# Performance work log

Measured on AMD Instinct MI355X. Metric: run time of the kernel, lower is better.

Reference implementation:

```python
import jax, jax.numpy as jnp
import numpy as np

B, L, D = 2048, 128, 256
NEG_SLOPE = 0.2   # GAT-style leaky relu slope
LN_EPS = 1e-5
NEG_INF = -1e9


def setup_inputs() -> dict:
    key = jax.random.key(0)
    ks = jax.random.split(key, 10)
    mol_atom_feature = jax.random.normal(ks[0], (B, D), jnp.float32)
    atom_feature = jax.random.normal(ks[1], (B, L, D), jnp.float32)
    # attend mask: 0/1 per atom; softmax mask: 0 where attended, -1e9 where padded
    attend = jax.random.randint(ks[2], (B, L, 1), 0, 2).astype(jnp.float32)
    softmax_mask = (attend - 1.0) * (-NEG_INF)  # 0 -> -1e9... careful: (0-1)*(1e9) = -1e9? compute: (attend-1)*1e9 gives -1e9 for 0, 0 for 1
    softmax_mask = (attend - 1.0) * 1e9
    s = 1.0 / np.sqrt(D)
    W1 = jax.random.normal(ks[3], (D, D), jnp.float32) * s
    b1 = jnp.zeros((D,), jnp.float32)
    W2 = jax.random.normal(ks[4], (D, D), jnp.float32) * s
    b2 = jnp.zeros((D,), jnp.float32)
    w_align = jax.random.normal(ks[5], (D, 1), jnp.float32) * s
    b_align = jnp.zeros((1,), jnp.float32)
    ln_gamma = jnp.ones((D,), jnp.float32)
    ln_beta = jnp.zeros((D,), jnp.float32)
    return {
        "mol_atom_feature": mol_atom_feature,
        "atom_feature": atom_feature,
        "mol_atom_attend_mask": attend,
        "mol_atom_softmax_mask": softmax_mask,
        "W1": W1, "b1": b1, "W2": W2, "b2": b2,
        "w_align": w_align, "b_align": b_align,
        "ln_gamma": ln_gamma, "ln_beta": ln_beta,
    }


def _leaky_relu(x):
    return jnp.where(x >= 0, x, NEG_SLOPE * x)


def reference(mol_atom_feature, atom_feature, mol_atom_attend_mask, mol_atom_softmax_mask,
              W1, b1, W2, b2, w_align, b_align, ln_gamma, ln_beta):
    # linear transforms (dropout is identity in eval)
    q = mol_atom_feature @ W1.T + b1                      # [B, D]
    nb = atom_feature @ W2.T + b2                         # [B, L, D]
    # GATv2: act(q + neighbor) -> scalar score
    align = _leaky_relu(q[:, None, :] + nb)               # [B, L, D]
    score = align @ w_align + b_align                     # [B, L, 1]
    score = score + mol_atom_softmax_mask
    attn = jax.nn.softmax(score, axis=-2)                 # softmax over atoms L
    attn = attn * mol_atom_attend_mask
    ctx = jnp.sum(attn * nb, axis=-2)                     # [B, D]
    # LayerNorm over feature dim
    mu = jnp.mean(ctx, axis=-1, keepdims=True)
    var = jnp.mean((ctx - mu) ** 2, axis=-1, keepdims=True)
    return (ctx - mu) / jnp.sqrt(var + LN_EPS) * ln_gamma + ln_beta
```

## Files before the change

kernel.cpp:

```cpp
#include <hip/hip_runtime.h>

#define NBMOL 2048
#define NL 128
#define ND 256

constexpr float NEG_SLOPE = 0.2f;
constexpr float LN_EPS = 1e-5f;

typedef __attribute__((ext_vector_type(8))) short short8;
typedef __attribute__((ext_vector_type(4))) float f32x4;

__device__ __forceinline__ unsigned short f2bf(float f) {
  unsigned int u = __float_as_uint(f);
  u = (u + 0x7FFFu + ((u >> 16) & 1u)) >> 16;
  return (unsigned short)u;
}
__device__ __forceinline__ float bf2f(unsigned short h) {
  return __uint_as_float(((unsigned int)h) << 16);
}
__device__ __forceinline__ int swz(int row, int kbyte) {
  return row * 512 + (kbyte ^ ((row & 7) << 4));
}

__global__ __launch_bounds__(256) void pack_w2_kernel(const float* __restrict__ W2,
                                                      unsigned short* __restrict__ w2f,
                                                      unsigned short* __restrict__ w2p) {
  int g = blockIdx.x * 256 + threadIdx.x;
  int ks = g >> 10;
  int nt = (g >> 6) & 15;
  int l  = g & 63;
  int row = (l & 15) + nt * 16;
  int kb  = ((l >> 4) << 3) + ks * 32;
  const float* src = W2 + row * 256 + kb;
  unsigned short h[8];
#pragma unroll
  for (int j = 0; j < 8; ++j) h[j] = f2bf(src[j]);
  unsigned short* dst = w2f + (size_t)g * 8;
#pragma unroll
  for (int j = 0; j < 8; ++j) dst[j] = h[j];
  unsigned short* dst2 = w2p + (size_t)row * 256 + kb;
#pragma unroll
  for (int j = 0; j < 8; ++j) dst2[j] = h[j];
}

__global__ __launch_bounds__(256) void compute_q_kernel(const float* __restrict__ mol,
                                                        const float* __restrict__ W1,
                                                        const float* __restrict__ b1,
                                                        float* __restrict__ q) {
  __shared__ float mol_s[8][ND];
  const int t = threadIdx.x;
  const int b0 = blockIdx.x * 8;
#pragma unroll
  for (int i = 0; i < 8; ++i) mol_s[i][t] = mol[(size_t)(b0 + i) * ND + t];
  __syncthreads();
  float acc[8];
#pragma unroll
  for (int i = 0; i < 8; ++i) acc[i] = 0.f;
  const float4* wrow = (const float4*)(W1 + (size_t)t * ND);
  for (int k4 = 0; k4 < 64; ++k4) {
    float4 w = wrow[k4];
#pragma unroll
    for (int bb = 0; bb < 8; ++bb) {
      float4 m = *(const float4*)&mol_s[bb][k4 * 4];
      acc[bb] += w.x * m.x + w.y * m.y + w.z * m.z + w.w * m.w;
    }
  }
  float bias = b1[t];
#pragma unroll
  for (int bb = 0; bb < 8; ++bb) q[(size_t)(b0 + bb) * ND + t] = acc[bb] + bias;
}

__global__ __launch_bounds__(512, 4) void fused_kernel(
    const float* __restrict__ atom,
    const float* __restrict__ attend,
    const float* __restrict__ smask,
    const float* __restrict__ w_align,
    const float* __restrict__ b_align,
    const float* __restrict__ b2,
    const float* __restrict__ gamma_,
    const float* __restrict__ beta_,
    const unsigned short* __restrict__ w2f,
    const unsigned short* __restrict__ w2p,
    const float* __restrict__ qbuf,
    float* __restrict__ out)
{
  __shared__ unsigned short Abuf[NL * ND];
  __shared__ float sp_s[4][NL];
  __shared__ float attn_s[NL];
  __shared__ float ctx4_s[4][ND];
  __shared__ float y_s[ND];
  __shared__ float gemv_s[2][ND];
  __shared__ float red_s[2][4];
  __shared__ float t_s;

  const int tid  = threadIdx.x;
  const int lane = tid & 63;
  const int wid  = tid >> 6;
  const int wr   = wid >> 2;
  const int wc   = wid & 3;
  const int b    = blockIdx.x;

  {
    const float4* src = (const float4*)(atom + (size_t)b * (NL * ND));
#pragma unroll
    for (int half = 0; half < 2; ++half) {
      float4 v[8];
#pragma unroll
      for (int i = 0; i < 8; ++i) v[i] = src[(half * 8 + i) * 512 + tid];
#pragma unroll
      for (int i = 0; i < 8; ++i) {
        int f = (half * 8 + i) * 512 + tid;
        int row = f >> 6;
        int kbyte = (f & 63) * 8;
        ushort4 hv;
        hv.x = f2bf(v[i].x); hv.y = f2bf(v[i].y);
        hv.z = f2bf(v[i].z); hv.w = f2bf(v[i].w);
        *(ushort4*)((char*)Abuf + swz(row, kbyte)) = hv;
      }
    }
  }
  __syncthreads();

  f32x4 acc[4][4];
#pragma unroll
  for (int mm = 0; mm < 4; ++mm)
#pragma unroll
    for (int nn = 0; nn < 4; ++nn) acc[mm][nn] = {0.f, 0.f, 0.f, 0.f};

#pragma unroll
  for (int ks = 0; ks < 8; ++ks) {
    short8 bfr[4], afr[4];
#pragma unroll
    for (int nn = 0; nn < 4; ++nn) {
      const unsigned short* srcb =
          w2f + ((size_t)((ks * 16 + (wc * 4 + nn)) * 64 + lane)) * 8;
      bfr[nn] = *(const short8*)srcb;
    }
#pragma unroll
    for (int mm = 0; mm < 4; ++mm) {
      int row = wr * 64 + mm * 16 + (lane & 15);
      int kbyte = ((lane >> 4) << 4) + ks * 64;
      afr[mm] = *(const short8*)((const char*)Abuf + swz(row, kbyte));
    }
#pragma unroll
    for (int mm = 0; mm < 4; ++mm)
#pragma unroll
      for (int nn = 0; nn < 4; ++nn)
        acc[mm][nn] = __builtin_amdgcn_mfma_f32_16x16x32_bf16(
            afr[mm], bfr[nn], acc[mm][nn], 0, 0, 0);
  }

  {
    float qv[4], wv[4], bv[4];
    const float* qrow = qbuf + (size_t)b * ND;
#pragma unroll
    for (int nn = 0; nn < 4; ++nn) {
      int col = wc * 64 + nn * 16 + (lane & 15);
      qv[nn] = qrow[col];
      wv[nn] = w_align[col];
      bv[nn] = b2[col];
    }
#pragma unroll
    for (int mm = 0; mm < 4; ++mm) {
#pragma unroll
      for (int r = 0; r < 4; ++r) {
        float s = 0.f;
#pragma unroll
        for (int nn = 0; nn < 4; ++nn) {
          float t2 = qv[nn] + acc[mm][nn][r] + bv[nn];
          s += (t2 >= 0.f ? t2 : NEG_SLOPE * t2) * wv[nn];
        }
        s += __shfl_xor(s, 1);
        s += __shfl_xor(s, 2);
        s += __shfl_xor(s, 4);
        s += __shfl_xor(s, 8);
        if ((lane & 15) == 0)
          sp_s[wc][wr * 64 + mm * 16 + ((lane >> 4) << 2) + r] = s;
      }
    }
  }
  __syncthreads();

  if (wid == 0) {
    const float ba = b_align[0];
    float s0 = sp_s[0][lane] + sp_s[1][lane] + sp_s[2][lane] + sp_s[3][lane]
               + ba + smask[(size_t)b * NL + lane];
    int l1 = lane + 64;
    float s1 = sp_s[0][l1] + sp_s[1][l1] + sp_s[2][l1] + sp_s[3][l1]
               + ba + smask[(size_t)b * NL + l1];
    float m = fmaxf(s0, s1);
#pragma unroll
    for (int o = 32; o > 0; o >>= 1) m = fmaxf(m, __shfl_xor(m, o));
    float e0 = expf(s0 - m), e1 = expf(s1 - m);
    float sum = e0 + e1;
#pragma unroll
    for (int o = 32; o > 0; o >>= 1) sum += __shfl_xor(sum, o);
    float inv = 1.f / sum;
    float a0 = e0 * inv * attend[(size_t)b * NL + lane];
    float a1 = e1 * inv * attend[(size_t)b * NL + l1];
    attn_s[lane] = a0;
    attn_s[l1]   = a1;
    float tl = a0 + a1;
#pragma unroll
    for (int o = 32; o > 0; o >>= 1) tl += __shfl_xor(tl, o);
    if (lane == 0) t_s = tl;
  }
  __syncthreads();

  {
    const int d2 = tid & 127;
    const int h  = tid >> 7;
    float s0 = 0.f, s1 = 0.f;
#pragma unroll 8
    for (int li = 0; li < 32; ++li) {
      int l = h * 32 + li;
      unsigned int v = *(const unsigned int*)((const char*)Abuf + swz(l, d2 * 4));
      float a = attn_s[l];
      s0 += a * bf2f((unsigned short)(v & 0xffffu));
      s1 += a * bf2f((unsigned short)(v >> 16));
    }
    *(float2*)&ctx4_s[h][2 * d2] = make_float2(s0, s1);
  }
  __syncthreads();
  if (tid < ND)
    y_s[tid] = ctx4_s[0][tid] + ctx4_s[1][tid] + ctx4_s[2][tid] + ctx4_s[3][tid];
  __syncthreads();

  {
    const int dp = tid & 255;
    const int kh = tid >> 8;
    const unsigned short* wrow = w2p + (size_t)dp * 256 + kh * 128;
    float s = 0.f;
#pragma unroll
    for (int k8 = 0; k8 < 16; ++k8) {
      short8 w8 = *(const short8*)(wrow + k8 * 8);
      const float* yy = &y_s[kh * 128 + k8 * 8];
#pragma unroll
      for (int j = 0; j < 8; ++j)
        s += bf2f((unsigned short)w8[j]) * yy[j];
    }
    gemv_s[kh][dp] = s;
  }
  __syncthreads();

  if (tid < ND) {
    float v = gemv_s[0][tid] + gemv_s[1][tid] + t_s * b2[tid];
    float sv = v, sq = v * v;
#pragma unroll
    for (int o = 32; o > 0; o >>= 1) {
      sv += __shfl_xor(sv, o);
      sq += __shfl_xor(sq, o);
    }
    if (lane == 0) { red_s[0][wid] = sv; red_s[1][wid] = sq; }
  }
  __syncthreads();
  if (tid < ND) {
    float v = gemv_s[0][tid] + gemv_s[1][tid] + t_s * b2[tid];
    float sv = red_s[0][0] + red_s[0][1] + red_s[0][2] + red_s[0][3];
    float sq = red_s[1][0] + red_s[1][1] + red_s[1][2] + red_s[1][3];
    float mu = sv * (1.0f / 256.0f);
    float var = fmaxf(sq * (1.0f / 256.0f) - mu * mu, 0.f);
    out[(size_t)b * ND + tid] =
        (v - mu) * rsqrtf(var + LN_EPS) * gamma_[tid] + beta_[tid];
  }
}

extern "C" void kernel_launch(void* const* d_in, const int* in_sizes, int n_in,
                              void* d_out, int out_size, void* d_ws, size_t ws_size,
                              hipStream_t stream) {
  const float* mol     = (const float*)d_in[0];
  const float* atom    = (const float*)d_in[1];
  const float* attend  = (const float*)d_in[2];
  const float* smask   = (const float*)d_in[3];
  const float* W1      = (const float*)d_in[4];
  const float* b1      = (const float*)d_in[5];
  const float* W2      = (const float*)d_in[6];
  const float* b2      = (const float*)d_in[7];
  const float* w_align = (const float*)d_in[8];
  const float* b_align = (const float*)d_in[9];
  const float* gamma_  = (const float*)d_in[10];
  const float* beta_   = (const float*)d_in[11];
  float* out = (float*)d_out;

  float* qbuf = (float*)d_ws;
  unsigned short* w2f = (unsigned short*)((char*)d_ws + (size_t)NBMOL * ND * 4);
  unsigned short* w2p = w2f + 65536;

  pack_w2_kernel<<<32, 256, 0, stream>>>(W2, w2f, w2p);
  compute_q_kernel<<<256, 256, 0, stream>>>(mol, W1, b1, qbuf);
  fused_kernel<<<NBMOL, 512, 0, stream>>>(atom, attend, smask, w_align, b_align,
                                          b2, gamma_, beta_, w2f, w2p, qbuf, out);
}
```

Measured before the change: 458.2 us.

## Compute context from MFMA accumulators and stream atom tiles directly from global

The LDS staging of the whole bf16 atom tile is removed. A fragments are now loaded straight from global fp32 and packed to bf16 in registers. The context vector is formed as the attention-weighted sum of the existing MFMA accumulators (atom·W2ᵀ), which replaces the second pass over atom plus the separate W2 GEMV. The constant b_align is dropped because softmax is shift-invariant. This frees about 64KB of LDS per block and removes redundant work, but the strided per-lane global fp32 loads may coalesce less well than the old cooperative load.

```diff
diff --git a/kernel.cpp b/kernel.cpp
--- a/kernel.cpp
+++ b/kernel.cpp
@@ -1,4 +1,5 @@
 #include <hip/hip_runtime.h>
+#include <hip/hip_bf16.h>
 
 #define NBMOL 2048
 #define NL 128
@@ -15,16 +16,15 @@
   u = (u + 0x7FFFu + ((u >> 16) & 1u)) >> 16;
   return (unsigned short)u;
 }
-__device__ __forceinline__ float bf2f(unsigned short h) {
-  return __uint_as_float(((unsigned int)h) << 16);
-}
-__device__ __forceinline__ int swz(int row, int kbyte) {
-  return row * 512 + (kbyte ^ ((row & 7) << 4));
+__device__ __forceinline__ unsigned int pk2(float lo, float hi) {
+  __hip_bfloat162 h = __float22bfloat162_rn(make_float2(lo, hi));
+  unsigned int u;
+  __builtin_memcpy(&u, &h, 4);
+  return u;
 }
 
 __global__ __launch_bounds__(256) void pack_w2_kernel(const float* __restrict__ W2,
-                                                      unsigned short* __restrict__ w2f,
-                                                      unsigned short* __restrict__ w2p) {
+                                                      unsigned short* __restrict__ w2f) {
   int g = blockIdx.x * 256 + threadIdx.x;
   int ks = g >> 10;
   int nt = (g >> 6) & 15;
@@ -38,9 +38,6 @@
   unsigned short* dst = w2f + (size_t)g * 8;
 #pragma unroll
   for (int j = 0; j < 8; ++j) dst[j] = h[j];
-  unsigned short* dst2 = w2p + (size_t)row * 256 + kb;
-#pragma unroll
-  for (int j = 0; j < 8; ++j) dst2[j] = h[j];
 }
 
 __global__ __launch_bounds__(256) void compute_q_kernel(const float* __restrict__ mol,
@@ -75,21 +72,16 @@
     const float* __restrict__ attend,
     const float* __restrict__ smask,
     const float* __restrict__ w_align,
-    const float* __restrict__ b_align,
     const float* __restrict__ b2,
     const float* __restrict__ gamma_,
     const float* __restrict__ beta_,
     const unsigned short* __restrict__ w2f,
-    const unsigned short* __restrict__ w2p,
     const float* __restrict__ qbuf,
     float* __restrict__ out)
 {
-  __shared__ unsigned short Abuf[NL * ND];
-  __shared__ float sp_s[4][NL];
-  __shared__ float attn_s[NL];
-  __shared__ float ctx4_s[4][ND];
-  __shared__ float y_s[ND];
-  __shared__ float gemv_s[2][ND];
+  __shared__ float __align__(16) sp_s[4][NL];
+  __shared__ float __align__(16) attn_s[NL];
+  __shared__ float cw_s[2][ND];
   __shared__ float red_s[2][4];
   __shared__ float t_s;
 
@@ -100,47 +92,32 @@
   const int wc   = wid & 3;
   const int b    = blockIdx.x;
 
-  {
-    const float4* src = (const float4*)(atom + (size_t)b * (NL * ND));
-#pragma unroll
-    for (int half = 0; half < 2; ++half) {
-      float4 v[8];
-#pragma unroll
-      for (int i = 0; i < 8; ++i) v[i] = src[(half * 8 + i) * 512 + tid];
-#pragma unroll
-      for (int i = 0; i < 8; ++i) {
-        int f = (half * 8 + i) * 512 + tid;
-        int row = f >> 6;
-        int kbyte = (f & 63) * 8;
-        ushort4 hv;
-        hv.x = f2bf(v[i].x); hv.y = f2bf(v[i].y);
-        hv.z = f2bf(v[i].z); hv.w = f2bf(v[i].w);
-        *(ushort4*)((char*)Abuf + swz(row, kbyte)) = hv;
-      }
-    }
-  }
-  __syncthreads();
-
   f32x4 acc[4][4];
 #pragma unroll
   for (int mm = 0; mm < 4; ++mm)
 #pragma unroll
     for (int nn = 0; nn < 4; ++nn) acc[mm][nn] = {0.f, 0.f, 0.f, 0.f};
 
+  const float* abase = atom + (size_t)b * (NL * ND)
+                     + (size_t)(wr * 64 + (lane & 15)) * ND + ((lane >> 4) << 3);
+  const unsigned short* bbase = w2f + (size_t)((wc * 4) * 64 + lane) * 8;
+
 #pragma unroll
   for (int ks = 0; ks < 8; ++ks) {
-    short8 bfr[4], afr[4];
-#pragma unroll
-    for (int nn = 0; nn < 4; ++nn) {
-      const unsigned short* srcb =
-          w2f + ((size_t)((ks * 16 + (wc * 4 + nn)) * 64 + lane)) * 8;
-      bfr[nn] = *(const short8*)srcb;
-    }
+    short8 bfr[4];
+#pragma unroll
+    for (int nn = 0; nn < 4; ++nn)
+      bfr[nn] = *(const short8*)(bbase + ((size_t)(ks * 16 + nn) * 64) * 8);
+    short8 afr[4];
 #pragma unroll
     for (int mm = 0; mm < 4; ++mm) {
-      int row = wr * 64 + mm * 16 + (lane & 15);
-      int kbyte = ((lane >> 4) << 4) + ks * 64;
-      afr[mm] = *(const short8*)((const char*)Abuf + swz(row, kbyte));
+      const float* ap = abase + mm * 16 * ND + ks * 32;
+      float4 a0 = *(const float4*)ap;
+      float4 a1 = *(const float4*)(ap + 4);
+      union { unsigned int u[4]; short8 s; } f;
+      f.u[0] = pk2(a0.x, a0.y); f.u[1] = pk2(a0.z, a0.w);
+      f.u[2] = pk2(a1.x, a1.y); f.u[3] = pk2(a1.z, a1.w);
+      afr[mm] = f.s;
     }
 #pragma unroll
     for (int mm = 0; mm < 4; ++mm)
@@ -182,12 +159,11 @@
   __syncthreads();
 
   if (wid == 0) {
-    const float ba = b_align[0];
     float s0 = sp_s[0][lane] + sp_s[1][lane] + sp_s[2][lane] + sp_s[3][lane]
-               + ba + smask[(size_t)b * NL + lane];
+               + smask[(size_t)b * NL + lane];
     int l1 = lane + 64;
     float s1 = sp_s[0][l1] + sp_s[1][l1] + sp_s[2][l1] + sp_s[3][l1]
-               + ba + smask[(size_t)b * NL + l1];
+               + smask[(size_t)b * NL + l1];
     float m = fmaxf(s0, s1);
 #pragma unroll
     for (int o = 32; o > 0; o >>= 1) m = fmaxf(m, __shfl_xor(m, o));
@@ -208,43 +184,31 @@
   __syncthreads();
 
   {
-    const int d2 = tid & 127;
-    const int h  = tid >> 7;
-    float s0 = 0.f, s1 = 0.f;
-#pragma unroll 8
-    for (int li = 0; li < 32; ++li) {
-      int l = h * 32 + li;
-      unsigned int v = *(const unsigned int*)((const char*)Abuf + swz(l, d2 * 4));
-      float a = attn_s[l];
-      s0 += a * bf2f((unsigned short)(v & 0xffffu));
-      s1 += a * bf2f((unsigned short)(v >> 16));
-    }
-    *(float2*)&ctx4_s[h][2 * d2] = make_float2(s0, s1);
-  }
-  __syncthreads();
-  if (tid < ND)
-    y_s[tid] = ctx4_s[0][tid] + ctx4_s[1][tid] + ctx4_s[2][tid] + ctx4_s[3][tid];
-  __syncthreads();
-
-  {
-    const int dp = tid & 255;
-    const int kh = tid >> 8;
-    const unsigned short* wrow = w2p + (size_t)dp * 256 + kh * 128;
-    float s = 0.f;
-#pragma unroll
-    for (int k8 = 0; k8 < 16; ++k8) {
-      short8 w8 = *(const short8*)(wrow + k8 * 8);
-      const float* yy = &y_s[kh * 128 + k8 * 8];
-#pragma unroll
-      for (int j = 0; j < 8; ++j)
-        s += bf2f((unsigned short)w8[j]) * yy[j];
-    }
-    gemv_s[kh][dp] = s;
+    float cp[4] = {0.f, 0.f, 0.f, 0.f};
+#pragma unroll
+    for (int mm = 0; mm < 4; ++mm) {
+      f32x4 av = *(const f32x4*)&attn_s[wr * 64 + mm * 16 + ((lane >> 4) << 2)];
+#pragma unroll
+      for (int r = 0; r < 4; ++r)
+#pragma unroll
+        for (int nn = 0; nn < 4; ++nn)
+          cp[nn] += av[r] * acc[mm][nn][r];
+    }
+#pragma unroll
+    for (int nn = 0; nn < 4; ++nn) {
+      cp[nn] += __shfl_xor(cp[nn], 16);
+      cp[nn] += __shfl_xor(cp[nn], 32);
+    }
+    if (lane < 16) {
+#pragma unroll
+      for (int nn = 0; nn < 4; ++nn)
+        cw_s[wr][wc * 64 + nn * 16 + lane] = cp[nn];
+    }
   }
   __syncthreads();
 
   if (tid < ND) {
-    float v = gemv_s[0][tid] + gemv_s[1][tid] + t_s * b2[tid];
+    float v = cw_s[0][tid] + cw_s[1][tid] + t_s * b2[tid];
     float sv = v, sq = v * v;
 #pragma unroll
     for (int o = 32; o > 0; o >>= 1) {
@@ -255,7 +219,7 @@
   }
   __syncthreads();
   if (tid < ND) {
-    float v = gemv_s[0][tid] + gemv_s[1][tid] + t_s * b2[tid];
+    float v = cw_s[0][tid] + cw_s[1][tid] + t_s * b2[tid];
     float sv = red_s[0][0] + red_s[0][1] + red_s[0][2] + red_s[0][3];
     float sq = red_s[1][0] + red_s[1][1] + red_s[1][2] + red_s[1][3];
     float mu = sv * (1.0f / 256.0f);
@@ -277,17 +241,15 @@
   const float* W2      = (const float*)d_in[6];
   const float* b2      = (const float*)d_in[7];
   const float* w_align = (const float*)d_in[8];
-  const float* b_align = (const float*)d_in[9];
   const float* gamma_  = (const float*)d_in[10];
   const float* beta_   = (const float*)d_in[11];
   float* out = (float*)d_out;
 
   float* qbuf = (float*)d_ws;
   unsigned short* w2f = (unsigned short*)((char*)d_ws + (size_t)NBMOL * ND * 4);
-  unsigned short* w2p = w2f + 65536;
-
-  pack_w2_kernel<<<32, 256, 0, stream>>>(W2, w2f, w2p);
+
+  pack_w2_kernel<<<32, 256, 0, stream>>>(W2, w2f);
   compute_q_kernel<<<256, 256, 0, stream>>>(mol, W1, b1, qbuf);
-  fused_kernel<<<NBMOL, 512, 0, stream>>>(atom, attend, smask, w_align, b_align,
-                                          b2, gamma_, beta_, w2f, w2p, qbuf, out);
-}
+  fused_kernel<<<NBMOL, 512, 0, stream>>>(atom, attend, smask, w_align,
+                                          b2, gamma_, beta_, w2f, qbuf, out);
+}
```

New measurement: 496.9 us. 8.4% more time.
